# Kernel optimization log

Measured on AMD Instinct MI355X. Metric: run time of the kernel, lower is better.

## Reference

```python
import jax, jax.numpy as jnp
import numpy as np

EXP = 2          # self.exp
NEG = -1e9       # mask fill value
B, N1, DIM, F = 4, 1024, 1024, 4
N = N1 + 1
NTOT = F * N     # 4100


def _normalize(x):
    # L2-normalize along last dim; also return the norm (keepdims)
    n = jnp.sqrt(jnp.sum(x * x, axis=-1, keepdims=True))
    return x / n, n


def setup_inputs() -> dict:
    key = jax.random.key(0)
    k1, k2 = jax.random.split(key)
    lhs = jax.random.normal(k1, (B, N1, DIM), dtype=jnp.float32)
    rhs = jax.random.normal(k2, (B, NTOT, DIM), dtype=jnp.float32)
    return {"lhs": lhs, "rhs": rhs}


def reference(lhs, rhs):
    b, n1, dim = lhs.shape
    n = n1 + 1
    ntot = rhs.shape[1]
    f = ntot // n

    lhs_n, lhs_norm = _normalize(lhs)          # (B,N1,D), (B,N1,1)
    rhs_n, _ = _normalize(rhs)                 # (B,Ntot,D)

    # cosine similarity GEMM + power epilogue
    sim = jnp.einsum('bnd,bmd->bnm', lhs_n, rhs_n) ** EXP   # (B,N1,Ntot)

    # view as (B, N1, F, N); torch masks:
    #   sim4[..., -N1:][~eye] = -1e9   (off-diagonal of last N1 cols)
    #   sim4[..., 0] = -1e9            (first col of each frame)
    # net keep condition: j == i + 1
    sim4 = sim.reshape(b, n1, f, n)
    i = jnp.arange(n1)[:, None, None]   # (N1,1,1)
    j = jnp.arange(n)[None, None, :]    # (1,1,N)
    keep = (j == i + 1)                 # (N1,1,N), broadcasts over F
    sim4 = jnp.where(keep, sim4, jnp.float32(NEG))

    return sim4.reshape(b, n1, ntot), lhs_norm
```

## Files before the change

### kernel.cpp

```cpp
#include <hip/hip_runtime.h>

#define BB   4
#define N1   1024
#define DIM  1024
#define FF   4
#define NN   1025
#define NTOT (FF * NN)
#define SIM_TOTAL ((size_t)BB * N1 * NTOT)
#define NEGV (-1e9f)

__global__ __launch_bounds__(256)
void fill_kernel(float4* __restrict__ out4, int total4) {
    const float4 negv = make_float4(NEGV, NEGV, NEGV, NEGV);
    const int stride = gridDim.x * 256;
    for (int k = blockIdx.x * 256 + threadIdx.x; k < total4; k += stride)
        out4[k] = negv;
}

__global__ __launch_bounds__(256)
void dot_kernel(const float* __restrict__ lhs,
                const float* __restrict__ rhs,
                float* __restrict__ out) {
    const int row  = blockIdx.x * 4 + (threadIdx.x >> 6);
    const int lane = threadIdx.x & 63;
    const int b    = row >> 10;
    const int i    = row & (N1 - 1);

    const float4* lrow = (const float4*)(lhs + (size_t)row * DIM);
    float4 lv[4];
#pragma unroll
    for (int k = 0; k < 4; ++k)
        lv[k] = lrow[lane + 64 * k];

    float l2 = 0.f;
#pragma unroll
    for (int k = 0; k < 4; ++k)
        l2 += lv[k].x * lv[k].x + lv[k].y * lv[k].y +
              lv[k].z * lv[k].z + lv[k].w * lv[k].w;

    float dotf[FF], r2f[FF];
#pragma unroll
    for (int f = 0; f < FF; ++f) {
        const size_t rrow_idx = (size_t)b * NTOT + (size_t)f * NN + (i + 1);
        const float4* rrow = (const float4*)(rhs + rrow_idx * DIM);
        float d = 0.f, r2 = 0.f;
#pragma unroll
        for (int k = 0; k < 4; ++k) {
            const float4 rv = rrow[lane + 64 * k];
            d  += lv[k].x * rv.x + lv[k].y * rv.y + lv[k].z * rv.z + lv[k].w * rv.w;
            r2 += rv.x * rv.x + rv.y * rv.y + rv.z * rv.z + rv.w * rv.w;
        }
        dotf[f] = d;
        r2f[f]  = r2;
    }

    float vals[9];
    vals[0] = l2;
#pragma unroll
    for (int f = 0; f < FF; ++f) {
        vals[1 + 2 * f] = dotf[f];
        vals[2 + 2 * f] = r2f[f];
    }
#pragma unroll
    for (int q = 0; q < 9; ++q) {
#pragma unroll
        for (int off = 1; off < 64; off <<= 1)
            vals[q] += __shfl_xor(vals[q], off, 64);
    }

    if (lane == 0) {
        const float L2 = vals[0];
        float* orow = out + (size_t)row * NTOT;
#pragma unroll
        for (int f = 0; f < FF; ++f) {
            const float d  = vals[1 + 2 * f];
            const float r2 = vals[2 + 2 * f];
            orow[f * NN + i + 1] = (d * d) / (L2 * r2);
        }
        out[SIM_TOTAL + row] = sqrtf(L2);
    }
}

extern "C" void kernel_launch(void* const* d_in, const int* in_sizes, int n_in,
                              void* d_out, int out_size, void* d_ws, size_t ws_size,
                              hipStream_t stream) {
    const float* lhs = (const float*)d_in[0];
    const float* rhs = (const float*)d_in[1];
    float* out = (float*)d_out;

    const int total4 = (int)(SIM_TOTAL / 4);
    fill_kernel<<<2048, 256, 0, stream>>>((float4*)out, total4);
    dot_kernel<<<(BB * N1) / 4, 256, 0, stream>>>(lhs, rhs, out);
}
```

Measured before the change: 134.7 us.

## Fuse mask fill into dot kernel with nontemporal vector row stores

Removes the separate -1e9 fill kernel. Each wavefront now writes its whole output row as float4 vectors, placing the four kept similarity values into that stream, so the output is written once from a single launch. All rhs loads are also hoisted ahead of the math to raise memory-level parallelism, and the shuffle reductions are interleaved. Nontemporal stores avoid polluting cache with the large output, but the grid of 1024 blocks may give less store parallelism than the dedicated fill kernel had.

```diff
diff --git a/kernel.cpp b/kernel.cpp
--- a/kernel.cpp
+++ b/kernel.cpp
@@ -9,16 +9,10 @@
 #define SIM_TOTAL ((size_t)BB * N1 * NTOT)
 #define NEGV (-1e9f)
 
-__global__ __launch_bounds__(256)
-void fill_kernel(float4* __restrict__ out4, int total4) {
-    const float4 negv = make_float4(NEGV, NEGV, NEGV, NEGV);
-    const int stride = gridDim.x * 256;
-    for (int k = blockIdx.x * 256 + threadIdx.x; k < total4; k += stride)
-        out4[k] = negv;
-}
+typedef float vfloat4 __attribute__((ext_vector_type(4)));
 
 __global__ __launch_bounds__(256)
-void dot_kernel(const float* __restrict__ lhs,
+void lcs_kernel(const float* __restrict__ lhs,
                 const float* __restrict__ rhs,
                 float* __restrict__ out) {
     const int row  = blockIdx.x * 4 + (threadIdx.x >> 6);
@@ -32,6 +26,16 @@
     for (int k = 0; k < 4; ++k)
         lv[k] = lrow[lane + 64 * k];
 
+    float4 rv[FF][4];
+#pragma unroll
+    for (int f = 0; f < FF; ++f) {
+        const float4* rrow = (const float4*)(rhs +
+            ((size_t)b * NTOT + (size_t)f * NN + (i + 1)) * DIM);
+#pragma unroll
+        for (int k = 0; k < 4; ++k)
+            rv[f][k] = rrow[lane + 64 * k];
+    }
+
     float l2 = 0.f;
 #pragma unroll
     for (int k = 0; k < 4; ++k)
@@ -41,44 +45,54 @@
     float dotf[FF], r2f[FF];
 #pragma unroll
     for (int f = 0; f < FF; ++f) {
-        const size_t rrow_idx = (size_t)b * NTOT + (size_t)f * NN + (i + 1);
-        const float4* rrow = (const float4*)(rhs + rrow_idx * DIM);
         float d = 0.f, r2 = 0.f;
 #pragma unroll
         for (int k = 0; k < 4; ++k) {
-            const float4 rv = rrow[lane + 64 * k];
-            d  += lv[k].x * rv.x + lv[k].y * rv.y + lv[k].z * rv.z + lv[k].w * rv.w;
-            r2 += rv.x * rv.x + rv.y * rv.y + rv.z * rv.z + rv.w * rv.w;
+            d  += lv[k].x * rv[f][k].x + lv[k].y * rv[f][k].y +
+                  lv[k].z * rv[f][k].z + lv[k].w * rv[f][k].w;
+            r2 += rv[f][k].x * rv[f][k].x + rv[f][k].y * rv[f][k].y +
+                  rv[f][k].z * rv[f][k].z + rv[f][k].w * rv[f][k].w;
         }
         dotf[f] = d;
         r2f[f]  = r2;
     }
 
-    float vals[9];
-    vals[0] = l2;
+#pragma unroll
+    for (int off = 1; off < 64; off <<= 1) {
+        l2 += __shfl_xor(l2, off, 64);
+#pragma unroll
+        for (int f = 0; f < FF; ++f) {
+            dotf[f] += __shfl_xor(dotf[f], off, 64);
+            r2f[f]  += __shfl_xor(r2f[f],  off, 64);
+        }
+    }
+
+    float sim[FF];
+    int   q[FF];
 #pragma unroll
     for (int f = 0; f < FF; ++f) {
-        vals[1 + 2 * f] = dotf[f];
-        vals[2 + 2 * f] = r2f[f];
-    }
-#pragma unroll
-    for (int q = 0; q < 9; ++q) {
-#pragma unroll
-        for (int off = 1; off < 64; off <<= 1)
-            vals[q] += __shfl_xor(vals[q], off, 64);
+        sim[f] = (dotf[f] * dotf[f]) / (l2 * r2f[f]);
+        q[f]   = f * NN + (i + 1);
     }
 
-    if (lane == 0) {
-        const float L2 = vals[0];
-        float* orow = out + (size_t)row * NTOT;
+    vfloat4* orow4 = (vfloat4*)(out + (size_t)row * NTOT);
+    for (int k = lane; k <= 1024; k += 64) {
+        const int g = 4 * k;
+        float v0 = NEGV, v1 = NEGV, v2 = NEGV, v3 = NEGV;
 #pragma unroll
         for (int f = 0; f < FF; ++f) {
-            const float d  = vals[1 + 2 * f];
-            const float r2 = vals[2 + 2 * f];
-            orow[f * NN + i + 1] = (d * d) / (L2 * r2);
+            v0 = (g + 0 == q[f]) ? sim[f] : v0;
+            v1 = (g + 1 == q[f]) ? sim[f] : v1;
+            v2 = (g + 2 == q[f]) ? sim[f] : v2;
+            v3 = (g + 3 == q[f]) ? sim[f] : v3;
         }
-        out[SIM_TOTAL + row] = sqrtf(L2);
+        vfloat4 v;
+        v.x = v0; v.y = v1; v.z = v2; v.w = v3;
+        __builtin_nontemporal_store(v, &orow4[k]);
     }
+
+    if (lane == 0)
+        out[SIM_TOTAL + row] = sqrtf(l2);
 }
 
 extern "C" void kernel_launch(void* const* d_in, const int* in_sizes, int n_in,
@@ -88,7 +102,5 @@
     const float* rhs = (const float*)d_in[1];
     float* out = (float*)d_out;
 
-    const int total4 = (int)(SIM_TOTAL / 4);
-    fill_kernel<<<2048, 256, 0, stream>>>((float4*)out, total4);
-    dot_kernel<<<(BB * N1) / 4, 256, 0, stream>>>(lhs, rhs, out);
+    lcs_kernel<<<(BB * N1) / 4, 256, 0, stream>>>(lhs, rhs, out);
 }
```

Result: faster. 129.6 us (-3.8%).
